# Kernel optimization log

Measured on AMD Instinct MI355X. Metric: run time of the kernel, lower is better.

## Reference

```python
import jax, jax.numpy as jnp
import numpy as np

N, E, F_IN, H = 50000, 800000, 500, 96

def setup_inputs() -> dict:
    key = jax.random.key(0)
    ks = jax.random.split(key, 10)
    x = jax.random.normal(ks[0], (N, F_IN), dtype=jnp.float32)
    src = jax.random.randint(ks[1], (E,), 0, N, dtype=jnp.int32)
    dst = jax.random.randint(ks[2], (E,), 0, N, dtype=jnp.int32)
    perm = jax.random.permutation(ks[3], N).astype(jnp.int32)
    W1 = jax.random.normal(ks[4], (F_IN, H), dtype=jnp.float32) / np.sqrt(F_IN)
    b1 = jnp.zeros((H,), jnp.float32)
    a1 = jnp.full((H,), 0.25, jnp.float32)  # PReLU init
    W2 = jax.random.normal(ks[5], (H, H), dtype=jnp.float32) / np.sqrt(H)
    b2 = jnp.zeros((H,), jnp.float32)
    a2 = jnp.full((H,), 0.25, jnp.float32)
    Wm = jax.random.normal(ks[6], (H, H), dtype=jnp.float32) / np.sqrt(H)
    bm = jnp.zeros((H,), jnp.float32)
    return {"x": x, "src": src, "dst": dst, "perm": perm,
            "W1": W1, "b1": b1, "a1": a1, "W2": W2, "b2": b2, "a2": a2,
            "Wm": Wm, "bm": bm}

def reference(x, src, dst, perm, W1, b1, a1, W2, b2, a2, Wm, bm):
    n = x.shape[0]
    ones = jnp.ones_like(src, dtype=x.dtype)
    deg_out = jnp.clip(jax.ops.segment_sum(ones, src, num_segments=n), 1.0)
    deg_in = jnp.clip(jax.ops.segment_sum(ones, dst, num_segments=n), 1.0)
    norm_out = (deg_out ** -0.5)[:, None]  # [N,1]
    norm_in = (deg_in ** -0.5)[:, None]

    def gconv(h, W, b, a):
        # DGL GraphConv, norm='both': D_out^-1/2 -> W -> A -> D_in^-1/2 -> +b -> PReLU
        h = (h * norm_out) @ W                                  # [N,H]
        agg = jax.ops.segment_sum(h[src], dst, num_segments=n)  # SpMM via gather/scatter
        h = agg * norm_in + b
        return jnp.where(h >= 0, h, a * h)                      # PReLU

    def encode(feat):
        h = gconv(feat, W1, b1, a1)
        return gconv(h, W2, b2, a2)

    z1 = encode(x)
    z2 = encode(x[perm])  # corrupted view: permuted node features
    z1 = z1 @ Wm + bm
    z2 = z2 @ Wm + bm
    return jnp.concatenate([z1.sum(1), z2.sum(1)], axis=0)  # [2N]
```

## Files before the change

kernel.cpp:

```cpp
#include <hip/hip_runtime.h>

#define H96 96

typedef __attribute__((ext_vector_type(8))) short bf16x8_t;
typedef __attribute__((ext_vector_type(4))) float f32x4_t;
typedef __attribute__((ext_vector_type(8))) _Float16 half8_t;

__global__ void deg8_kernel(const int* __restrict__ src, const int* __restrict__ dst,
                            int* __restrict__ d8, int E, int NP8) {
    int e = blockIdx.x * blockDim.x + threadIdx.x;
    int c = blockIdx.x & 7;
    if (e < E) {
        int* base = d8 + (size_t)c * 2 * NP8;
        atomicAdd(base + src[e], 1);
        atomicAdd(base + NP8 + dst[e], 1);
    }
}

__global__ void degred_kernel(const int* __restrict__ d8, int* __restrict__ deg_in,
                              float* __restrict__ no, float* __restrict__ ni,
                              int N, int NP8) {
    int i = blockIdx.x * 256 + threadIdx.x;
    if (i >= N) return;
    int so = 0, si = 0;
#pragma unroll
    for (int c = 0; c < 8; c++) {
        so += d8[(size_t)c * 2 * NP8 + i];
        si += d8[(size_t)c * 2 * NP8 + NP8 + i];
    }
    deg_in[i] = si;
    no[i] = rsqrtf(fmaxf((float)so, 1.0f));
    ni[i] = rsqrtf(fmaxf((float)si, 1.0f));
}

__global__ void scanA_kernel(const int* __restrict__ in, int* __restrict__ pre,
                             int* __restrict__ bsums, int n) {
    __shared__ int s[256];
    int i = blockIdx.x * 256 + threadIdx.x;
    int v = (i < n) ? in[i] : 0;
    s[threadIdx.x] = v;
    __syncthreads();
    for (int off = 1; off < 256; off <<= 1) {
        int t = (threadIdx.x >= off) ? s[threadIdx.x - off] : 0;
        __syncthreads();
        s[threadIdx.x] += t;
        __syncthreads();
    }
    if (i < n) pre[i] = s[threadIdx.x] - v;
    if (threadIdx.x == 255) bsums[blockIdx.x] = s[255];
}

__global__ void scanB_kernel(int* __restrict__ bsums, int nb) {
    __shared__ int s[256];
    int v = (threadIdx.x < nb) ? bsums[threadIdx.x] : 0;
    s[threadIdx.x] = v;
    __syncthreads();
    for (int off = 1; off < 256; off <<= 1) {
        int t = (threadIdx.x >= off) ? s[threadIdx.x - off] : 0;
        __syncthreads();
        s[threadIdx.x] += t;
        __syncthreads();
    }
    if (threadIdx.x < nb) bsums[threadIdx.x] = s[threadIdx.x] - v;
}

__global__ void rowfin_kernel(const int* __restrict__ pre, const int* __restrict__ bsums,
                              int* __restrict__ row_start, int* __restrict__ cursor,
                              int N, int E) {
    int i = blockIdx.x * 256 + threadIdx.x;
    if (i < N) {
        int v = pre[i] + bsums[blockIdx.x];
        row_start[i] = v;
        cursor[i] = v;
    }
    if (i == 0) row_start[N] = E;
}

__global__ void scatter_kernel(const int* __restrict__ src, const int* __restrict__ dst,
                               const int* __restrict__ perm, const float* __restrict__ norm_out,
                               int* __restrict__ cursor, int4* __restrict__ edge4, int E) {
    int e = blockIdx.x * 256 + threadIdx.x;
    if (e < E) {
        int d = dst[e];
        int s = src[e];
        int p = atomicAdd(cursor + d, 1);
        edge4[p] = make_int4(s, perm[s], __float_as_int(norm_out[s]), 0);
    }
}

__global__ void histblk_kernel(const int* __restrict__ deg, int* __restrict__ hb,
                               int N, int nb) {
    __shared__ int h[256];
    h[threadIdx.x] = 0;
    __syncthreads();
    int i = blockIdx.x * 256 + threadIdx.x;
    if (i < N) atomicAdd(&h[min(deg[i], 255)], 1);
    __syncthreads();
    hb[threadIdx.x * nb + blockIdx.x] = h[threadIdx.x];
}

__global__ void place2_kernel(const int* __restrict__ deg, const int* __restrict__ hpre,
                              const int* __restrict__ bsums, int* __restrict__ order,
                              int N, int nb) {
    __shared__ int cur[256];
    int idx = threadIdx.x * nb + blockIdx.x;
    cur[threadIdx.x] = hpre[idx] + bsums[idx >> 8];
    __syncthreads();
    int i = blockIdx.x * 256 + threadIdx.x;
    if (i < N) {
        int b = min(deg[i], 255);
        int p = atomicAdd(&cur[b], 1);
        order[p] = i;
    }
}

__device__ __forceinline__ void f2bf2(float v, unsigned short& h, unsigned short& l) {
    unsigned int b = __float_as_uint(v);
    unsigned short hh = (unsigned short)((b + 0x7FFFu + ((b >> 16) & 1u)) >> 16);
    float fh = __uint_as_float(((unsigned int)hh) << 16);
    float r = v - fh;
    unsigned int rb = __float_as_uint(r);
    unsigned short ll = (unsigned short)((rb + 0x7FFFu + ((rb >> 16) & 1u)) >> 16);
    h = hh; l = ll;
}

__device__ __forceinline__ void cvt8(const float f[8], bf16x8_t& ah, bf16x8_t& al) {
    union { unsigned int u[4]; bf16x8_t v; } H, L;
#pragma unroll
    for (int i = 0; i < 4; i++) {
        float v0 = f[2 * i], v1 = f[2 * i + 1];
        unsigned int b0 = __float_as_uint(v0);
        unsigned int b1 = __float_as_uint(v1);
        unsigned int m0 = b0 & 0xFFFF0000u;
        unsigned int m1 = b1 & 0xFFFF0000u;
        float r0 = v0 - __uint_as_float(m0);
        float r1 = v1 - __uint_as_float(m1);
        H.u[i] = (b0 >> 16) | m1;
        L.u[i] = (__float_as_uint(r0) >> 16) | (__float_as_uint(r1) & 0xFFFF0000u);
    }
    ah = H.v; al = L.v;
}

__global__ void weights_prep(const float* __restrict__ W1, const float* __restrict__ W2,
                             const float* __restrict__ Wm, const float* __restrict__ bm,
                             unsigned short* __restrict__ w1h, unsigned short* __restrict__ w1l,
                             unsigned short* __restrict__ w2h, unsigned short* __restrict__ w2l,
                             float* __restrict__ wsum, float* __restrict__ bsum,
                             int F, int KP1) {
    int idx = blockIdx.x * 256 + threadIdx.x;
    int z1 = 96 * KP1, z2 = z1 + 96 * 96;
    if (idx < z1) {
        int n = idx / KP1, k = idx - n * KP1;
        float v = (k < F) ? W1[(size_t)k * 96 + n] : 0.f;
        unsigned short h, l;
        f2bf2(v, h, l);
        w1h[idx] = h; w1l[idx] = l;
    } else if (idx < z2) {
        int t = idx - z1;
        int n = t / 96, k = t - n * 96;
        float v = W2[(size_t)k * 96 + n];
        unsigned short h, l;
        f2bf2(v, h, l);
        w2h[t] = h; w2l[t] = l;
    } else if (idx < z2 + 96) {
        int c = idx - z2;
        float s = 0.f;
        for (int j = 0; j < 96; j++) s += Wm[c * 96 + j];
        wsum[c] = s;
    } else if (idx == z2 + 96) {
        float s = 0.f;
        for (int j = 0; j < 96; j++) s += bm[j];
        bsum[0] = s;
    }
}

#define GBM 64
#define GBK 32

__device__ __forceinline__ void gload_lds16(const void* g, void* l) {
    __builtin_amdgcn_global_load_lds(
        (const __attribute__((address_space(1))) unsigned int*)g,
        (__attribute__((address_space(3))) unsigned int*)l, 16, 0, 0);
}

template<int AH>
__global__ __launch_bounds__(256, 6) void gemm_mfma(const void* __restrict__ Av,
                                                    const unsigned short* __restrict__ Bth,
                                                    const unsigned short* __restrict__ Btl,
                                                    _Float16* __restrict__ C16,
                                                    int M, int K, int KP) {
    __shared__ alignas(16) unsigned short Bs[2][2][96][4][8];
    int tid = threadIdx.x;
    int wid = tid >> 6, lane = tid & 63;
    int q = lane >> 4, mn = lane & 15;
    int row0 = blockIdx.x * GBM + wid * 16;
    int arow = min(row0 + mn, M - 1);
    int nk = (K + GBK - 1) / GBK;

    const float* A32 = (const float*)Av;
    const _Float16* A16 = (const _Float16*)Av;

    const unsigned short* gsrc[3];
    int lbase[3];
#pragma unroll
    for (int i = 0; i < 3; i++) {
        int c = wid * 192 + i * 64 + lane;
        int part = (c >= 384) ? 1 : 0;
        int rem = c - part * 384;
        int row = rem >> 2, slot = rem & 3;
        int kc = slot ^ ((row >> 1) & 3);
        gsrc[i] = (part ? Btl : Bth) + (size_t)row * KP + kc * 8;
        lbase[i] = (wid * 192 + i * 64) * 8;
    }

    auto stage = [&](int t, int buf) {
#pragma unroll
        for (int i = 0; i < 3; i++)
            gload_lds16(gsrc[i] + (size_t)t * GBK, &Bs[buf][0][0][0][0] + lbase[i]);
    };

    auto loadA = [&](int t, float* f) {
        int gk = t * GBK + q * 8;
        if (AH) {
            uint4 raw = *(const uint4*)(A16 + (size_t)arow * K + gk);
            const _Float16* hp = (const _Float16*)&raw;
#pragma unroll
            for (int c = 0; c < 8; c++) f[c] = (float)hp[c];
        } else {
            if (gk + 8 <= K) {
                float4 v0 = *(const float4*)(A32 + (size_t)arow * K + gk);
                float4 v1 = *(const float4*)(A32 + (size_t)arow * K + gk + 4);
                f[0] = v0.x; f[1] = v0.y; f[2] = v0.z; f[3] = v0.w;
                f[4] = v1.x; f[5] = v1.y; f[6] = v1.z; f[7] = v1.w;
            } else {
#pragma unroll
                for (int c = 0; c < 8; c++)
                    f[c] = (gk + c < K) ? A32[(size_t)arow * K + gk + c] : 0.f;
            }
        }
    };

    f32x4_t acc[6] = {};
    float f[8], fn[8];

    stage(0, 0);
    loadA(0, f);

    int slotR = q ^ ((mn >> 1) & 3);

    for (int t = 0; t < nk; t++) {
        int tn = (t + 1 < nk) ? t + 1 : nk - 1;
        stage(tn, (t + 1) & 1);
        loadA(tn, fn);
        if (AH) asm volatile("s_waitcnt vmcnt(4)" ::: "memory");
        else    asm volatile("s_waitcnt vmcnt(5)" ::: "memory");
        __builtin_amdgcn_sched_barrier(0);
        __builtin_amdgcn_s_barrier();

        bf16x8_t ah, al;
        cvt8(f, ah, al);

        const unsigned short* bp = &Bs[t & 1][0][0][0][0] + mn * 32 + slotR * 8;
#pragma unroll
        for (int ct = 0; ct < 6; ct++) {
            bf16x8_t bh = *(const bf16x8_t*)(bp + ct * 512);
            bf16x8_t bl = *(const bf16x8_t*)(bp + 3072 + ct * 512);
            acc[ct] = __builtin_amdgcn_mfma_f32_16x16x32_bf16(ah, bh, acc[ct], 0, 0, 0);
            acc[ct] = __builtin_amdgcn_mfma_f32_16x16x32_bf16(ah, bl, acc[ct], 0, 0, 0);
            acc[ct] = __builtin_amdgcn_mfma_f32_16x16x32_bf16(al, bh, acc[ct], 0, 0, 0);
        }
        asm volatile("s_waitcnt lgkmcnt(0)" ::: "memory");
        __builtin_amdgcn_sched_barrier(0);
        __builtin_amdgcn_s_barrier();

#pragma unroll
        for (int c = 0; c < 8; c++) f[c] = fn[c];
    }

    asm volatile("s_waitcnt vmcnt(0)" ::: "memory");
    __builtin_amdgcn_sched_barrier(0);

#pragma unroll
    for (int reg = 0; reg < 4; reg++) {
        int gr = row0 + q * 4 + reg;
        if (gr < M) {
#pragma unroll
            for (int ct = 0; ct < 6; ct++)
                C16[(size_t)gr * H96 + ct * 16 + mn] = (_Float16)acc[ct][reg];
        }
    }
}

__device__ __forceinline__ void fmah8(float4& a, float4& b, float s, half8_t v) {
    a.x = fmaf(s, (float)v[0], a.x); a.y = fmaf(s, (float)v[1], a.y);
    a.z = fmaf(s, (float)v[2], a.z); a.w = fmaf(s, (float)v[3], a.w);
    b.x = fmaf(s, (float)v[4], b.x); b.y = fmaf(s, (float)v[5], b.y);
    b.z = fmaf(s, (float)v[6], b.z); b.w = fmaf(s, (float)v[7], b.w);
}

__device__ __forceinline__ float4 prelu4(float4 acc, float ni, float4 b, float4 a) {
    float4 h;
    h.x = fmaf(acc.x, ni, b.x); h.x = (h.x >= 0.f) ? h.x : a.x * h.x;
    h.y = fmaf(acc.y, ni, b.y); h.y = (h.y >= 0.f) ? h.y : a.y * h.y;
    h.z = fmaf(acc.z, ni, b.z); h.z = (h.z >= 0.f) ? h.z : a.z * h.z;
    h.w = fmaf(acc.w, ni, b.w); h.w = (h.w >= 0.f) ? h.w : a.w * h.w;
    return h;
}

__global__ __launch_bounds__(384) void spmm1_dual(
        const half8_t* __restrict__ yh, const int* __restrict__ row_start,
        const int4* __restrict__ edge4, const int* __restrict__ order,
        const float* __restrict__ norm_out, const float* __restrict__ norm_in,
        const float* __restrict__ b1, const float* __restrict__ a1,
        half8_t* __restrict__ h1, half8_t* __restrict__ h2, int N) {
    int g = blockIdx.x * 32 + threadIdx.y;
    if (g >= N) return;
    int d = order[g];
    int tx = threadIdx.x;
    int beg = row_start[d], end = row_start[d + 1];
    const half8_t* yt = yh + tx;
    float4 a1a = {0,0,0,0}, a1b = {0,0,0,0}, a2a = {0,0,0,0}, a2b = {0,0,0,0};
    int j = beg;
    for (; j + 8 <= end; j += 8) {
        int4 e[8];
#pragma unroll
        for (int q = 0; q < 8; q++) e[q] = edge4[j + q];
        half8_t u[8], w[8];
#pragma unroll
        for (int q = 0; q < 8; q++) u[q] = yt[(size_t)e[q].x * 12];
#pragma unroll
        for (int q = 0; q < 8; q++) w[q] = yt[(size_t)e[q].y * 12];
#pragma unroll
        for (int q = 0; q < 8; q++) {
            float n = __int_as_float(e[q].z);
            fmah8(a1a, a1b, n, u[q]);
            fmah8(a2a, a2b, n, w[q]);
        }
    }
    for (; j < end; j++) {
        int4 e = edge4[j];
        float n = __int_as_float(e.z);
        fmah8(a1a, a1b, n, yt[(size_t)e.x * 12]);
        fmah8(a2a, a2b, n, yt[(size_t)e.y * 12]);
    }
    float ni = norm_in[d], no = norm_out[d];
    float4 bb0 = ((const float4*)b1)[tx * 2], bb1 = ((const float4*)b1)[tx * 2 + 1];
    float4 aa0 = ((const float4*)a1)[tx * 2], aa1 = ((const float4*)a1)[tx * 2 + 1];
    float4 r1a = prelu4(a1a, ni, bb0, aa0), r1b = prelu4(a1b, ni, bb1, aa1);
    float4 r2a = prelu4(a2a, ni, bb0, aa0), r2b = prelu4(a2b, ni, bb1, aa1);
    half8_t o1, o2;
    o1[0] = (_Float16)(r1a.x * no); o1[1] = (_Float16)(r1a.y * no);
    o1[2] = (_Float16)(r1a.z * no); o1[3] = (_Float16)(r1a.w * no);
    o1[4] = (_Float16)(r1b.x * no); o1[5] = (_Float16)(r1b.y * no);
    o1[6] = (_Float16)(r1b.z * no); o1[7] = (_Float16)(r1b.w * no);
    o2[0] = (_Float16)(r2a.x * no); o2[1] = (_Float16)(r2a.y * no);
    o2[2] = (_Float16)(r2a.z * no); o2[3] = (_Float16)(r2a.w * no);
    o2[4] = (_Float16)(r2b.x * no); o2[5] = (_Float16)(r2b.y * no);
    o2[6] = (_Float16)(r2b.z * no); o2[7] = (_Float16)(r2b.w * no);
    h1[(size_t)d * 12 + tx] = o1;
    h2[(size_t)d * 12 + tx] = o2;
}

__global__ __launch_bounds__(384) void spmm2_dual(
        const half8_t* __restrict__ th,
        const int* __restrict__ row_start, const int4* __restrict__ edge4,
        const int* __restrict__ order, const float* __restrict__ norm_in,
        const float* __restrict__ b2, const float* __restrict__ a2,
        const float* __restrict__ wsum, const float* __restrict__ bsum,
        float* __restrict__ outp, int N) {
    int g = blockIdx.x * 32 + threadIdx.y;
    int tx = threadIdx.x;
    int ty = threadIdx.y;
    bool valid = (g < N);
    int d = valid ? order[g] : 0;
    int beg = 0, end = 0;
    if (valid) { beg = row_start[d]; end = row_start[d + 1]; }
    const half8_t* t1 = th + tx;
    const half8_t* t2 = th + (size_t)N * 12 + tx;
    float4 a1a = {0,0,0,0}, a1b = {0,0,0,0}, a2a = {0,0,0,0}, a2b = {0,0,0,0};
    int j = beg;
    for (; j + 8 <= end; j += 8) {
        int s[8];
#pragma unroll
        for (int q = 0; q < 8; q++) s[q] = edge4[j + q].x;
        half8_t u[8], w[8];
#pragma unroll
        for (int q = 0; q < 8; q++) u[q] = t1[(size_t)s[q] * 12];
#pragma unroll
        for (int q = 0; q < 8; q++) w[q] = t2[(size_t)s[q] * 12];
#pragma unroll
        for (int q = 0; q < 8; q++) {
            fmah8(a1a, a1b, 1.f, u[q]);
            fmah8(a2a, a2b, 1.f, w[q]);
        }
    }
    for (; j < end; j++) {
        int s = edge4[j].x;
        fmah8(a1a, a1b, 1.f, t1[(size_t)s * 12]);
        fmah8(a2a, a2b, 1.f, t2[(size_t)s * 12]);
    }
    float ni = valid ? norm_in[d] : 0.f;
    float4 bb0 = ((const float4*)b2)[tx * 2], bb1 = ((const float4*)b2)[tx * 2 + 1];
    float4 aa0 = ((const float4*)a2)[tx * 2], aa1 = ((const float4*)a2)[tx * 2 + 1];
    float4 wv0 = ((const float4*)wsum)[tx * 2], wv1 = ((const float4*)wsum)[tx * 2 + 1];
    float4 r1a = prelu4(a1a, ni, bb0, aa0), r1b = prelu4(a1b, ni, bb1, aa1);
    float4 r2a = prelu4(a2a, ni, bb0, aa0), r2b = prelu4(a2b, ni, bb1, aa1);
    float p1 = r1a.x * wv0.x + r1a.y * wv0.y + r1a.z * wv0.z + r1a.w * wv0.w
             + r1b.x * wv1.x + r1b.y * wv1.y + r1b.z * wv1.z + r1b.w * wv1.w;
    float p2 = r2a.x * wv0.x + r2a.y * wv0.y + r2a.z * wv0.z + r2a.w * wv0.w
             + r2b.x * wv1.x + r2b.y * wv1.y + r2b.z * wv1.z + r2b.w * wv1.w;
    __shared__ float red1[32][12];
    __shared__ float red2[32][12];
    red1[ty][tx] = p1;
    red2[ty][tx] = p2;
    __syncthreads();
    if (tx == 0 && valid) {
        float s1 = 0.f, s2 = 0.f;
#pragma unroll
        for (int k = 0; k < 12; k++) { s1 += red1[ty][k]; s2 += red2[ty][k]; }
        outp[d] = s1 + bsum[0];
        outp[N + d] = s2 + bsum[0];
    }
}

extern "C" void kernel_launch(void* const* d_in, const int* in_sizes, int n_in,
                              void* d_out, int out_size, void* d_ws, size_t ws_size,
                              hipStream_t stream) {
    const float* x    = (const float*)d_in[0];
    const int*   src  = (const int*)d_in[1];
    const int*   dst  = (const int*)d_in[2];
    const int*   perm = (const int*)d_in[3];
    const float* W1   = (const float*)d_in[4];
    const float* b1   = (const float*)d_in[5];
    const float* a1   = (const float*)d_in[6];
    const float* W2   = (const float*)d_in[7];
    const float* b2   = (const float*)d_in[8];
    const float* a2   = (const float*)d_in[9];
    const float* Wm   = (const float*)d_in[10];
    const float* bm   = (const float*)d_in[11];
    float* out = (float*)d_out;

    int E = in_sizes[1];
    int N = in_sizes[3];
    int F = in_sizes[0] / N;
    int KP1 = ((F + GBK - 1) / GBK) * GBK;

    size_t NP = ((size_t)N + 256) & ~(size_t)255;
    size_t EP = ((size_t)E + 255) & ~(size_t)255;
    int nb = (N + 255) / 256;
    size_t HB = ((size_t)256 * nb + 255) & ~(size_t)255;

    int* deg_out   = (int*)d_ws;
    int* deg_in    = deg_out + NP;
    int* pre       = deg_in + NP;
    int* row_start = pre + NP;
    int* cursor    = row_start + NP;
    int* order     = cursor + NP;
    int* bsums     = order + NP;
    int* hb        = bsums + 256;
    int* hpre      = hb + HB;
    int4* edge4    = (int4*)(hpre + HB);
    float* norm_out = (float*)(edge4 + EP);
    float* norm_in  = norm_out + NP;
    float* wsum     = norm_in + NP;
    float* bsum     = wsum + 128;
    unsigned short* w1th = (unsigned short*)(bsum + 128);
    unsigned short* w1tl = w1th + 49664;
    unsigned short* w2th = w1tl + 49664;
    unsigned short* w2tl = w2th + 9728;
    _Float16* yh  = (_Float16*)(w2tl + 9728);
    _Float16* h1h = yh + ((size_t)N * H96 + 256);
    _Float16* th  = h1h + ((size_t)2 * N * H96 + 256);

    int* d8 = (int*)edge4;

    hipMemsetAsync(d8, 0, 16 * NP * sizeof(int), stream);
    deg8_kernel<<<(E + 255) / 256, 256, 0, stream>>>(src, dst, d8, E, (int)NP);
    degred_kernel<<<(N + 255) / 256, 256, 0, stream>>>(d8, deg_in, norm_out, norm_in,
                                                       N, (int)NP);

    scanA_kernel<<<nb, 256, 0, stream>>>(deg_in, pre, bsums, N);
    scanB_kernel<<<1, 256, 0, stream>>>(bsums, nb);
    rowfin_kernel<<<nb, 256, 0, stream>>>(pre, bsums, row_start, cursor, N, E);
    scatter_kernel<<<(E + 255) / 256, 256, 0, stream>>>(src, dst, perm, norm_out, cursor,
                                                        edge4, E);

    histblk_kernel<<<nb, 256, 0, stream>>>(deg_in, hb, N, nb);
    int n2 = 256 * nb;
    int nb2 = (n2 + 255) / 256;
    scanA_kernel<<<nb2, 256, 0, stream>>>(hb, hpre, bsums, n2);
    scanB_kernel<<<1, 256, 0, stream>>>(bsums, nb2);
    place2_kernel<<<nb, 256, 0, stream>>>(deg_in, hpre, bsums, order, N, nb);

    int wtot = 96 * KP1 + 96 * 96 + 96 + 1;
    weights_prep<<<(wtot + 255) / 256, 256, 0, stream>>>(W1, W2, Wm, bm, w1th, w1tl,
                                                         w2th, w2tl, wsum, bsum, F, KP1);

    gemm_mfma<0><<<(N + GBM - 1) / GBM, 256, 0, stream>>>(x, w1th, w1tl, yh, N, F, KP1);

    int nsb = (N + 31) / 32;
    spmm1_dual<<<nsb, dim3(12, 32), 0, stream>>>(
        (const half8_t*)yh, row_start, edge4, order, norm_out, norm_in,
        b1, a1, (half8_t*)h1h, (half8_t*)(h1h + (size_t)N * H96), N);

    gemm_mfma<1><<<(2 * N + GBM - 1) / GBM, 256, 0, stream>>>(h1h, w2th, w2tl, th, 2 * N, H96, H96);

    spmm2_dual<<<nsb, dim3(12, 32), 0, stream>>>(
        (const half8_t*)th, row_start, edge4, order, norm_in, b2, a2,
        wsum, bsum, out, N);
}
```

Measured before the change: 444.0 us.

## Interleave clean and permuted features per node to halve gather row fetches

The first GEMM now writes each projected row twice into an interleaved [N,192] buffer: once in the clean half of its own row and once in the permuted half of the row given by the inverse permutation. Both SpMM kernels can then fetch the clean and corrupted views of a neighbour from one contiguous 384-byte row instead of two scattered rows. The edge record shrinks from int4 to int2 because the permuted source index is no longer needed. The cost is an extra inverse-permutation kernel and a scattered second store in the GEMM epilogue. The second GEMM's output reuses the first buffer, which keeps the same interleaved layout as its hpair input.

```diff
diff --git a/kernel.cpp b/kernel.cpp
--- a/kernel.cpp
+++ b/kernel.cpp
@@ -31,6 +31,11 @@
     deg_in[i] = si;
     no[i] = rsqrtf(fmaxf((float)so, 1.0f));
     ni[i] = rsqrtf(fmaxf((float)si, 1.0f));
+}
+
+__global__ void iperm_kernel(const int* __restrict__ perm, int* __restrict__ iperm, int N) {
+    int i = blockIdx.x * 256 + threadIdx.x;
+    if (i < N) iperm[perm[i]] = i;
 }
 
 __global__ void scanA_kernel(const int* __restrict__ in, int* __restrict__ pre,
@@ -77,14 +82,14 @@
 }
 
 __global__ void scatter_kernel(const int* __restrict__ src, const int* __restrict__ dst,
-                               const int* __restrict__ perm, const float* __restrict__ norm_out,
-                               int* __restrict__ cursor, int4* __restrict__ edge4, int E) {
+                               const float* __restrict__ norm_out,
+                               int* __restrict__ cursor, int2* __restrict__ edge2, int E) {
     int e = blockIdx.x * 256 + threadIdx.x;
     if (e < E) {
         int d = dst[e];
         int s = src[e];
         int p = atomicAdd(cursor + d, 1);
-        edge4[p] = make_int4(s, perm[s], __float_as_int(norm_out[s]), 0);
+        edge2[p] = make_int2(s, __float_as_int(norm_out[s]));
     }
 }
 
@@ -188,6 +193,7 @@
                                                     const unsigned short* __restrict__ Bth,
                                                     const unsigned short* __restrict__ Btl,
                                                     _Float16* __restrict__ C16,
+                                                    const int* __restrict__ ipermArr,
                                                     int M, int K, int KP) {
     __shared__ alignas(16) unsigned short Bs[2][2][96][4][8];
     int tid = threadIdx.x;
@@ -284,9 +290,19 @@
     for (int reg = 0; reg < 4; reg++) {
         int gr = row0 + q * 4 + reg;
         if (gr < M) {
-#pragma unroll
-            for (int ct = 0; ct < 6; ct++)
-                C16[(size_t)gr * H96 + ct * 16 + mn] = (_Float16)acc[ct][reg];
+            if (AH) {
+#pragma unroll
+                for (int ct = 0; ct < 6; ct++)
+                    C16[(size_t)gr * H96 + ct * 16 + mn] = (_Float16)acc[ct][reg];
+            } else {
+                int ip = ipermArr[gr];
+#pragma unroll
+                for (int ct = 0; ct < 6; ct++) {
+                    _Float16 v = (_Float16)acc[ct][reg];
+                    C16[(size_t)gr * 192 + ct * 16 + mn] = v;
+                    C16[(size_t)ip * 192 + 96 + ct * 16 + mn] = v;
+                }
+            }
         }
     }
 }
@@ -308,40 +324,40 @@
 }
 
 __global__ __launch_bounds__(384) void spmm1_dual(
-        const half8_t* __restrict__ yh, const int* __restrict__ row_start,
-        const int4* __restrict__ edge4, const int* __restrict__ order,
+        const half8_t* __restrict__ yp, const int* __restrict__ row_start,
+        const int2* __restrict__ edge2, const int* __restrict__ order,
         const float* __restrict__ norm_out, const float* __restrict__ norm_in,
         const float* __restrict__ b1, const float* __restrict__ a1,
-        half8_t* __restrict__ h1, half8_t* __restrict__ h2, int N) {
+        half8_t* __restrict__ hpair, int N) {
     int g = blockIdx.x * 32 + threadIdx.y;
     if (g >= N) return;
     int d = order[g];
     int tx = threadIdx.x;
     int beg = row_start[d], end = row_start[d + 1];
-    const half8_t* yt = yh + tx;
+    const half8_t* yt = yp + tx;
     float4 a1a = {0,0,0,0}, a1b = {0,0,0,0}, a2a = {0,0,0,0}, a2b = {0,0,0,0};
     int j = beg;
     for (; j + 8 <= end; j += 8) {
-        int4 e[8];
-#pragma unroll
-        for (int q = 0; q < 8; q++) e[q] = edge4[j + q];
+        int2 e[8];
+#pragma unroll
+        for (int q = 0; q < 8; q++) e[q] = edge2[j + q];
         half8_t u[8], w[8];
 #pragma unroll
-        for (int q = 0; q < 8; q++) u[q] = yt[(size_t)e[q].x * 12];
-#pragma unroll
-        for (int q = 0; q < 8; q++) w[q] = yt[(size_t)e[q].y * 12];
+        for (int q = 0; q < 8; q++) u[q] = yt[(size_t)e[q].x * 24];
+#pragma unroll
+        for (int q = 0; q < 8; q++) w[q] = yt[(size_t)e[q].x * 24 + 12];
 #pragma unroll
         for (int q = 0; q < 8; q++) {
-            float n = __int_as_float(e[q].z);
+            float n = __int_as_float(e[q].y);
             fmah8(a1a, a1b, n, u[q]);
             fmah8(a2a, a2b, n, w[q]);
         }
     }
     for (; j < end; j++) {
-        int4 e = edge4[j];
-        float n = __int_as_float(e.z);
-        fmah8(a1a, a1b, n, yt[(size_t)e.x * 12]);
-        fmah8(a2a, a2b, n, yt[(size_t)e.y * 12]);
+        int2 e = edge2[j];
+        float n = __int_as_float(e.y);
+        fmah8(a1a, a1b, n, yt[(size_t)e.x * 24]);
+        fmah8(a2a, a2b, n, yt[(size_t)e.x * 24 + 12]);
     }
     float ni = norm_in[d], no = norm_out[d];
     float4 bb0 = ((const float4*)b1)[tx * 2], bb1 = ((const float4*)b1)[tx * 2 + 1];
@@ -357,13 +373,13 @@
     o2[2] = (_Float16)(r2a.z * no); o2[3] = (_Float16)(r2a.w * no);
     o2[4] = (_Float16)(r2b.x * no); o2[5] = (_Float16)(r2b.y * no);
     o2[6] = (_Float16)(r2b.z * no); o2[7] = (_Float16)(r2b.w * no);
-    h1[(size_t)d * 12 + tx] = o1;
-    h2[(size_t)d * 12 + tx] = o2;
+    hpair[(size_t)d * 24 + tx] = o1;
+    hpair[(size_t)d * 24 + 12 + tx] = o2;
 }
 
 __global__ __launch_bounds__(384) void spmm2_dual(
         const half8_t* __restrict__ th,
-        const int* __restrict__ row_start, const int4* __restrict__ edge4,
+        const int* __restrict__ row_start, const int2* __restrict__ edge2,
         const int* __restrict__ order, const float* __restrict__ norm_in,
         const float* __restrict__ b2, const float* __restrict__ a2,
         const float* __restrict__ wsum, const float* __restrict__ bsum,
@@ -376,18 +392,17 @@
     int beg = 0, end = 0;
     if (valid) { beg = row_start[d]; end = row_start[d + 1]; }
     const half8_t* t1 = th + tx;
-    const half8_t* t2 = th + (size_t)N * 12 + tx;
     float4 a1a = {0,0,0,0}, a1b = {0,0,0,0}, a2a = {0,0,0,0}, a2b = {0,0,0,0};
     int j = beg;
     for (; j + 8 <= end; j += 8) {
         int s[8];
 #pragma unroll
-        for (int q = 0; q < 8; q++) s[q] = edge4[j + q].x;
+        for (int q = 0; q < 8; q++) s[q] = edge2[j + q].x;
         half8_t u[8], w[8];
 #pragma unroll
-        for (int q = 0; q < 8; q++) u[q] = t1[(size_t)s[q] * 12];
-#pragma unroll
-        for (int q = 0; q < 8; q++) w[q] = t2[(size_t)s[q] * 12];
+        for (int q = 0; q < 8; q++) u[q] = t1[(size_t)s[q] * 24];
+#pragma unroll
+        for (int q = 0; q < 8; q++) w[q] = t1[(size_t)s[q] * 24 + 12];
 #pragma unroll
         for (int q = 0; q < 8; q++) {
             fmah8(a1a, a1b, 1.f, u[q]);
@@ -395,9 +410,9 @@
         }
     }
     for (; j < end; j++) {
-        int s = edge4[j].x;
-        fmah8(a1a, a1b, 1.f, t1[(size_t)s * 12]);
-        fmah8(a2a, a2b, 1.f, t2[(size_t)s * 12]);
+        int s = edge2[j].x;
+        fmah8(a1a, a1b, 1.f, t1[(size_t)s * 24]);
+        fmah8(a2a, a2b, 1.f, t1[(size_t)s * 24 + 12]);
     }
     float ni = valid ? norm_in[d] : 0.f;
     float4 bb0 = ((const float4*)b2)[tx * 2], bb1 = ((const float4*)b2)[tx * 2 + 1];
@@ -450,8 +465,8 @@
     int nb = (N + 255) / 256;
     size_t HB = ((size_t)256 * nb + 255) & ~(size_t)255;
 
-    int* deg_out   = (int*)d_ws;
-    int* deg_in    = deg_out + NP;
+    int* iperm     = (int*)d_ws;
+    int* deg_in    = iperm + NP;
     int* pre       = deg_in + NP;
     int* row_start = pre + NP;
     int* cursor    = row_start + NP;
@@ -459,8 +474,8 @@
     int* bsums     = order + NP;
     int* hb        = bsums + 256;
     int* hpre      = hb + HB;
-    int4* edge4    = (int4*)(hpre + HB);
-    float* norm_out = (float*)(edge4 + EP);
+    int2* edge2    = (int2*)(hpre + HB);
+    float* norm_out = (float*)(edge2 + EP);
     float* norm_in  = norm_out + NP;
     float* wsum     = norm_in + NP;
     float* bsum     = wsum + 128;
@@ -468,22 +483,25 @@
     unsigned short* w1tl = w1th + 49664;
     unsigned short* w2th = w1tl + 49664;
     unsigned short* w2tl = w2th + 9728;
-    _Float16* yh  = (_Float16*)(w2tl + 9728);
-    _Float16* h1h = yh + ((size_t)N * H96 + 256);
-    _Float16* th  = h1h + ((size_t)2 * N * H96 + 256);
-
-    int* d8 = (int*)edge4;
+    _Float16* fpA = (_Float16*)(w2tl + 9728);
+    _Float16* fpB = fpA + ((size_t)N * 192 + 256);
+    _Float16* ypair = fpA;
+    _Float16* hpair = fpB;
+    _Float16* th    = fpA;
+
+    int* d8 = (int*)edge2;
 
     hipMemsetAsync(d8, 0, 16 * NP * sizeof(int), stream);
     deg8_kernel<<<(E + 255) / 256, 256, 0, stream>>>(src, dst, d8, E, (int)NP);
     degred_kernel<<<(N + 255) / 256, 256, 0, stream>>>(d8, deg_in, norm_out, norm_in,
                                                        N, (int)NP);
+    iperm_kernel<<<(N + 255) / 256, 256, 0, stream>>>(perm, iperm, N);
 
     scanA_kernel<<<nb, 256, 0, stream>>>(deg_in, pre, bsums, N);
     scanB_kernel<<<1, 256, 0, stream>>>(bsums, nb);
     rowfin_kernel<<<nb, 256, 0, stream>>>(pre, bsums, row_start, cursor, N, E);
-    scatter_kernel<<<(E + 255) / 256, 256, 0, stream>>>(src, dst, perm, norm_out, cursor,
-                                                        edge4, E);
+    scatter_kernel<<<(E + 255) / 256, 256, 0, stream>>>(src, dst, norm_out, cursor,
+                                                        edge2, E);
 
     histblk_kernel<<<nb, 256, 0, stream>>>(deg_in, hb, N, nb);
     int n2 = 256 * nb;
@@ -496,16 +514,18 @@
     weights_prep<<<(wtot + 255) / 256, 256, 0, stream>>>(W1, W2, Wm, bm, w1th, w1tl,
                                                          w2th, w2tl, wsum, bsum, F, KP1);
 
-    gemm_mfma<0><<<(N + GBM - 1) / GBM, 256, 0, stream>>>(x, w1th, w1tl, yh, N, F, KP1);
+    gemm_mfma<0><<<(N + GBM - 1) / GBM, 256, 0, stream>>>(x, w1th, w1tl, ypair, iperm,
+                                                          N, F, KP1);
 
     int nsb = (N + 31) / 32;
     spmm1_dual<<<nsb, dim3(12, 32), 0, stream>>>(
-        (const half8_t*)yh, row_start, edge4, order, norm_out, norm_in,
-        b1, a1, (half8_t*)h1h, (half8_t*)(h1h + (size_t)N * H96), N);
-
-    gemm_mfma<1><<<(2 * N + GBM - 1) / GBM, 256, 0, stream>>>(h1h, w2th, w2tl, th, 2 * N, H96, H96);
+        (const half8_t*)ypair, row_start, edge2, order, norm_out, norm_in,
+        b1, a1, (half8_t*)hpair, N);
+
+    gemm_mfma<1><<<(2 * N + GBM - 1) / GBM, 256, 0, stream>>>(hpair, w2th, w2tl, th,
+                                                              nullptr, 2 * N, H96, H96);
 
     spmm2_dual<<<nsb, dim3(12, 32), 0, stream>>>(
-        (const half8_t*)th, row_start, edge4, order, norm_in, b2, a2,
+        (const half8_t*)th, row_start, edge2, order, norm_in, b2, a2,
         wsum, bsum, out, N);
 }
```

Measured after the change: 440.1 us. Within noise of the previous version (-0.9%).
